# Kernel tuning notes

Measured on AMD Instinct MI355X. Metric: run time of the kernel, lower is better.

Reference implementation:

```python
import jax, jax.numpy as jnp
import numpy as np

N_NODES = 20000
N_EDGES = 200000
D_IN, D_H1, D_H2, D_OUT = 1433, 1000, 500, 7


def setup_inputs() -> dict:
    key = jax.random.key(0)
    ks = jax.random.split(key, 8)
    features = jax.random.normal(ks[0], (N_NODES, D_IN), dtype=jnp.float32)
    src = jax.random.randint(ks[1], (N_EDGES,), 0, N_NODES)
    dst = jax.random.randint(ks[2], (N_EDGES,), 0, N_NODES)
    W1 = jax.random.normal(ks[3], (D_IN, D_H1), dtype=jnp.float32) * 0.02
    b1 = jnp.zeros((D_H1,), dtype=jnp.float32)
    W2 = jax.random.normal(ks[4], (D_H1, D_H2), dtype=jnp.float32) * 0.02
    b2 = jnp.zeros((D_H2,), dtype=jnp.float32)
    W3 = jax.random.normal(ks[5], (D_H2, D_OUT), dtype=jnp.float32) * 0.02
    b3 = jnp.zeros((D_OUT,), dtype=jnp.float32)
    return {"features": features, "src": src, "dst": dst,
            "W1": W1, "b1": b1, "W2": W2, "b2": b2, "W3": W3, "b3": b3}


def reference(features, src, dst, W1, b1, W2, b2, W3, b3):
    N = features.shape[0]

    def agg(x):  # sum_tensors over incoming neighbors: h_i = sum_{(j->i) in E} x_j
        return jax.ops.segment_sum(x[src], dst, num_segments=N)

    # GCN layer 1: aggregate -> linear -> relu
    x = jax.nn.relu(agg(features) @ W1 + b1)       # [N, 1000]
    # GCN layer 2: aggregate -> linear -> relu (dropout = identity in eval)
    x = jax.nn.relu(agg(x) @ W2 + b2)              # [N, 500]
    # output linear -> relu (dropout = identity in eval)
    x = jax.nn.relu(x @ W3 + b3)                   # [N, 7]
    return x
```

## Files before the change

kernel.cpp:

```cpp
#include <hip/hip_runtime.h>
#include <hip/hip_bf16.h>


#define N_NODES 20000
#define N_EDGES 200000
#define D_IN    1433
#define D_H1    1000
#define D_H2    500
#define D_OUT   7

#define MPAD    20096
#define K1PAD   1472
#define N1PAD   1024
#define K2PAD   1024
#define N2PAD   512
#define H1STR   1008
#define H2STR   504
#define MBLK    157

typedef __attribute__((ext_vector_type(8))) short short8;
typedef __attribute__((ext_vector_type(8))) unsigned short ushort8_t;
typedef __attribute__((ext_vector_type(4))) float f32x4;

__device__ __forceinline__ unsigned short bf16_rne(float x) {
    unsigned int u = __float_as_uint(x);
    u = (u + 0x7FFFu + ((u >> 16) & 1u)) >> 16;
    return (unsigned short)u;
}
__device__ __forceinline__ float bf16_up(unsigned short h) {
    return __uint_as_float((unsigned int)h << 16);
}

__device__ __forceinline__ void gl_lds16(const unsigned short* g, unsigned short* lds) {
    __builtin_amdgcn_global_load_lds(
        (const __attribute__((address_space(1))) unsigned int*)g,
        (__attribute__((address_space(3))) unsigned int*)lds, 16, 0, 0);
}

__global__ __launch_bounds__(256) void count_deg(const int* __restrict__ dst,
                                                 int* __restrict__ offs) {
    int e = blockIdx.x * 256 + threadIdx.x;
    if (e < N_EDGES) atomicAdd(&offs[dst[e] + 1], 1);
}

__global__ __launch_bounds__(1024) void scan_csr(int* __restrict__ offs,
                                                 int* __restrict__ cursor, int n) {
    __shared__ int wsum[16];
    __shared__ int s_carry;
    const int t = threadIdx.x, lane = t & 63, wv = t >> 6;
    if (t == 0) s_carry = 0;
    __syncthreads();
    for (int base = 0; base < n; base += 1024) {
        int i = base + t;
        int v = (i < n) ? offs[i] : 0;
        #pragma unroll
        for (int s = 1; s < 64; s <<= 1) {
            int u = __shfl_up(v, s, 64);
            if (lane >= s) v += u;
        }
        if (lane == 63) wsum[wv] = v;
        __syncthreads();
        int prefix = s_carry;
        for (int k = 0; k < wv; ++k) prefix += wsum[k];
        v += prefix;
        if (i < n) {
            offs[i] = v;
            if (i < N_NODES) cursor[i] = v;
        }
        __syncthreads();
        if (t == 1023) s_carry = v;
    }
}

__global__ __launch_bounds__(256) void fill_csr(const int* __restrict__ src,
                                                const int* __restrict__ dst,
                                                int* __restrict__ cursor,
                                                int* __restrict__ srcs) {
    int e = blockIdx.x * 256 + threadIdx.x;
    if (e < N_EDGES) {
        int pos = atomicAdd(&cursor[dst[e]], 1);
        srcs[pos] = src[e];
    }
}

__global__ __launch_bounds__(256) void cast_features(const float* __restrict__ F,
                                                     unsigned int* __restrict__ out) {
    int row = blockIdx.x;
    int t = threadIdx.x;
    const float* fr = F + (size_t)row * D_IN;
    bool live = row < N_NODES;
    for (int kk = t; kk < K1PAD / 2; kk += 256) {
        int k0 = kk * 2;
        float a = (live && k0     < D_IN) ? fr[k0]     : 0.f;
        float b = (live && k0 + 1 < D_IN) ? fr[k0 + 1] : 0.f;
        out[(size_t)row * (K1PAD / 2) + kk] =
            (unsigned int)bf16_rne(a) | ((unsigned int)bf16_rne(b) << 16);
    }
}

template <int SR, int SC, int DR, int DC>
__global__ __launch_bounds__(256) void transpose_cast_pad(const float* __restrict__ src,
                                                          unsigned short* __restrict__ dst) {
    __shared__ float tile[32][33];
    int c0 = blockIdx.x * 32;
    int r0 = blockIdx.y * 32;
    int tx = threadIdx.x & 31, ty = threadIdx.x >> 5;
    #pragma unroll
    for (int p = 0; p < 4; ++p) {
        int r = r0 + ty + p * 8, c = c0 + tx;
        tile[ty + p * 8][tx] = (r < SR && c < SC) ? src[(size_t)r * SC + c] : 0.f;
    }
    __syncthreads();
    #pragma unroll
    for (int p = 0; p < 4; ++p) {
        int dr = c0 + ty + p * 8;
        int dc = r0 + tx;
        if (dr < DR && dc < DC) dst[(size_t)dr * DC + dc] = bf16_rne(tile[tx][ty + p * 8]);
    }
}

template <int KPAD, int NB>
__global__ __launch_bounds__(256) void gemm_mfma(const unsigned short* __restrict__ A,
                                                 const unsigned short* __restrict__ B,
                                                 unsigned short* __restrict__ C,
                                                 int M, int N, int OSTR) {
    __shared__ __align__(16) unsigned short sA[128 * 64];
    __shared__ __align__(16) unsigned short sB[128 * 64];
    const int bid = blockIdx.x;
    const int xcd = bid & 7;
    const int tt  = bid >> 3;
    const int nb  = tt % NB;
    const int mb  = (tt / NB) * 8 + xcd;
    if (mb >= MBLK) return;

    const int t = threadIdx.x;
    const int w = t >> 6, lane = t & 63;
    const int m0 = mb * 128, n0 = nb * 128;
    const int wm = (w >> 1) * 64, wn = (w & 1) * 64;

    const int srowo = lane >> 3;
    const int skc   = ((lane & 7) ^ srowo) * 8;
    const int mrow = lane & 15, quad = lane >> 4;

    const unsigned short* Aptr = A + (size_t)(m0 + srowo) * KPAD + skc;
    const unsigned short* Bptr = B + (size_t)(n0 + srowo) * KPAD + skc;

    f32x4 acc[4][4] = {};

    for (int k0 = 0; k0 < KPAD; k0 += 64) {
        #pragma unroll
        for (int c = 0; c < 4; ++c) {
            const int rbase = c * 32 + w * 8;
            gl_lds16(Aptr + (size_t)rbase * KPAD, &sA[rbase * 64]);
            gl_lds16(Bptr + (size_t)rbase * KPAD, &sB[rbase * 64]);
        }
        Aptr += 64; Bptr += 64;
        __syncthreads();

        #pragma unroll
        for (int s = 0; s < 2; ++s) {
            short8 af[4], bf[4];
            #pragma unroll
            for (int mt = 0; mt < 4; ++mt) {
                int r = wm + mt * 16 + mrow;
                af[mt] = *(const short8*)&sA[r * 64 + (((s * 4 + quad) ^ (mrow & 7)) * 8)];
            }
            #pragma unroll
            for (int nt = 0; nt < 4; ++nt) {
                int r = wn + nt * 16 + mrow;
                bf[nt] = *(const short8*)&sB[r * 64 + (((s * 4 + quad) ^ (mrow & 7)) * 8)];
            }
            #pragma unroll
            for (int mt = 0; mt < 4; ++mt)
                #pragma unroll
                for (int nt = 0; nt < 4; ++nt)
                    acc[mt][nt] = __builtin_amdgcn_mfma_f32_16x16x32_bf16(
                        af[mt], bf[nt], acc[mt][nt], 0, 0, 0);
        }
        __syncthreads();
    }

    #pragma unroll
    for (int mt = 0; mt < 4; ++mt) {
        int m = m0 + wm + mt * 16 + quad * 4;
        #pragma unroll
        for (int nt = 0; nt < 4; ++nt) {
            int n = n0 + wn + nt * 16 + mrow;
            if (n >= N) continue;
            #pragma unroll
            for (int r = 0; r < 4; ++r)
                if (m + r < M) C[(size_t)(m + r) * OSTR + n] = bf16_rne(acc[mt][nt][r]);
        }
    }
}

__global__ __launch_bounds__(128) void agg1_bf16(const unsigned short* __restrict__ H,
                                                 const int* __restrict__ offs,
                                                 const int* __restrict__ srcs,
                                                 const float* __restrict__ bias,
                                                 unsigned short* __restrict__ X) {
    const int i = blockIdx.x, t = threadIdx.x;
    const bool active = t < 125;
    const int tc = active ? t : 124;
    ushort8_t o = (ushort8_t)0;
    if (i < N_NODES) {
        const int beg = offs[i], end = offs[i + 1];
        const unsigned short* Hc = H + tc * 8;
        float s[8] = {};
        int e = beg;
        for (; e + 4 <= end; e += 4) {
            int j0 = srcs[e], j1 = srcs[e + 1], j2 = srcs[e + 2], j3 = srcs[e + 3];
            ushort8_t v0 = *(const ushort8_t*)(Hc + (size_t)j0 * H1STR);
            ushort8_t v1 = *(const ushort8_t*)(Hc + (size_t)j1 * H1STR);
            ushort8_t v2 = *(const ushort8_t*)(Hc + (size_t)j2 * H1STR);
            ushort8_t v3 = *(const ushort8_t*)(Hc + (size_t)j3 * H1STR);
            #pragma unroll
            for (int u = 0; u < 8; ++u)
                s[u] += (bf16_up(v0[u]) + bf16_up(v1[u])) +
                        (bf16_up(v2[u]) + bf16_up(v3[u]));
        }
        for (; e < end; ++e) {
            ushort8_t v = *(const ushort8_t*)(Hc + (size_t)srcs[e] * H1STR);
            #pragma unroll
            for (int u = 0; u < 8; ++u) s[u] += bf16_up(v[u]);
        }
        if (active) {
            #pragma unroll
            for (int u = 0; u < 8; ++u)
                o[u] = bf16_rne(fmaxf(s[u] + bias[t * 8 + u], 0.f));
        }
    }
    *(ushort8_t*)(X + (size_t)i * K2PAD + t * 8) = o;
}

__global__ __launch_bounds__(128) void agg2_out(const unsigned short* __restrict__ H,
                                                const int* __restrict__ offs,
                                                const int* __restrict__ srcs,
                                                const float* __restrict__ b2,
                                                const float* __restrict__ W3,
                                                const float* __restrict__ b3,
                                                float* __restrict__ out) {
    __shared__ float red[2][8];
    const int i = blockIdx.x, t = threadIdx.x;
    const bool active = t < 125;
    const int tc = active ? t : 124;
    const int beg = offs[i], end = offs[i + 1];
    const unsigned short* Hc = H + tc * 4;
    float s[4] = {};
    int e = beg;
    for (; e + 4 <= end; e += 4) {
        int j0 = srcs[e], j1 = srcs[e + 1], j2 = srcs[e + 2], j3 = srcs[e + 3];
        ushort4 v0 = *(const ushort4*)(Hc + (size_t)j0 * H2STR);
        ushort4 v1 = *(const ushort4*)(Hc + (size_t)j1 * H2STR);
        ushort4 v2 = *(const ushort4*)(Hc + (size_t)j2 * H2STR);
        ushort4 v3 = *(const ushort4*)(Hc + (size_t)j3 * H2STR);
        s[0] += (bf16_up(v0.x) + bf16_up(v1.x)) + (bf16_up(v2.x) + bf16_up(v3.x));
        s[1] += (bf16_up(v0.y) + bf16_up(v1.y)) + (bf16_up(v2.y) + bf16_up(v3.y));
        s[2] += (bf16_up(v0.z) + bf16_up(v1.z)) + (bf16_up(v2.z) + bf16_up(v3.z));
        s[3] += (bf16_up(v0.w) + bf16_up(v1.w)) + (bf16_up(v2.w) + bf16_up(v3.w));
    }
    for (; e < end; ++e) {
        ushort4 v = *(const ushort4*)(Hc + (size_t)srcs[e] * H2STR);
        s[0] += bf16_up(v.x); s[1] += bf16_up(v.y);
        s[2] += bf16_up(v.z); s[3] += bf16_up(v.w);
    }
    float acc[D_OUT] = {};
    if (active) {
        #pragma unroll
        for (int u = 0; u < 4; ++u) {
            float x = fmaxf(s[u] + b2[t * 4 + u], 0.f);
            const float* wr = W3 + (size_t)(t * 4 + u) * D_OUT;
            #pragma unroll
            for (int j = 0; j < D_OUT; ++j) acc[j] += x * wr[j];
        }
    }
    #pragma unroll
    for (int j = 0; j < D_OUT; ++j)
        #pragma unroll
        for (int off = 32; off; off >>= 1) acc[j] += __shfl_down(acc[j], off);
    const int lane = t & 63, wave = t >> 6;
    if (lane == 0) {
        #pragma unroll
        for (int j = 0; j < D_OUT; ++j) red[wave][j] = acc[j];
    }
    __syncthreads();
    if (t == 0) {
        #pragma unroll
        for (int j = 0; j < D_OUT; ++j)
            out[(size_t)i * D_OUT + j] = fmaxf(red[0][j] + red[1][j] + b3[j], 0.f);
    }
}

extern "C" void kernel_launch(void* const* d_in, const int* in_sizes, int n_in,
                              void* d_out, int out_size, void* d_ws, size_t ws_size,
                              hipStream_t stream) {
    const float* features = (const float*)d_in[0];
    const int*   src      = (const int*)d_in[1];
    const int*   dst      = (const int*)d_in[2];
    const float* W1       = (const float*)d_in[3];
    const float* b1       = (const float*)d_in[4];
    const float* W2       = (const float*)d_in[5];
    const float* b2       = (const float*)d_in[6];
    const float* W3       = (const float*)d_in[7];
    const float* b3       = (const float*)d_in[8];
    float* out = (float*)d_out;

    char* ws = (char*)d_ws;
    unsigned short* Fbf  = (unsigned short*)(ws + 0);
    unsigned short* X1bf = (unsigned short*)(ws + 0);
    unsigned short* H1   = (unsigned short*)(ws + 59162624);
    unsigned short* H2   = (unsigned short*)(ws + 59162624);
    unsigned short* W1T  = (unsigned short*)(ws + 99482624);
    unsigned short* W2T  = (unsigned short*)(ws + 102497280);
    int* offs   = (int*)(ws + 103545856);
    int* cursor = (int*)(ws + 103625984);
    int* srcs   = (int*)(ws + 103706112);

    hipMemsetAsync(offs, 0, (N_NODES + 1) * sizeof(int), stream);
    count_deg<<<(N_EDGES + 255) / 256, 256, 0, stream>>>(dst, offs);
    scan_csr<<<1, 1024, 0, stream>>>(offs, cursor, N_NODES + 1);
    fill_csr<<<(N_EDGES + 255) / 256, 256, 0, stream>>>(src, dst, cursor, srcs);

    cast_features<<<MPAD, 256, 0, stream>>>(features, (unsigned int*)Fbf);
    transpose_cast_pad<D_IN, D_H1, N1PAD, K1PAD>
        <<<dim3(N1PAD / 32, K1PAD / 32), 256, 0, stream>>>(W1, W1T);
    transpose_cast_pad<D_H1, D_H2, N2PAD, K2PAD>
        <<<dim3(N2PAD / 32, K2PAD / 32), 256, 0, stream>>>(W2, W2T);

    gemm_mfma<K1PAD, N1PAD / 128><<<8 * (N1PAD / 128) * 20, 256, 0, stream>>>(
        Fbf, W1T, H1, N_NODES, D_H1, H1STR);
    agg1_bf16<<<MPAD, 128, 0, stream>>>(H1, offs, srcs, b1, X1bf);

    gemm_mfma<K2PAD, N2PAD / 128><<<8 * (N2PAD / 128) * 20, 256, 0, stream>>>(
        X1bf, W2T, H2, N_NODES, D_H2, H2STR);
    agg2_out<<<N_NODES, 128, 0, stream>>>(H2, offs, srcs, b2, W3, b3, out);
}
```

Measured before the change: 439.3 us.

## Fuse CSR scan, feature cast and weight transposes into one prep launch; fold fill into GEMM1

Merges the feature cast, both weight transpose-casts and the CSR prefix scan into a single multi-role prep kernel selected by block index. The scan now runs in a single 256-thread block instead of 1024 threads. The CSR fill runs as extra blocks appended to the first GEMM launch. This removes several kernel launches and their serialization gaps, but the scan block may become a long tail because it has fewer threads and runs alongside the other prep work.

After: 448.9 us. +2.2%, slower.

```diff
diff --git a/kernel.cpp b/kernel.cpp
--- a/kernel.cpp
+++ b/kernel.cpp
@@ -43,67 +43,15 @@
     if (e < N_EDGES) atomicAdd(&offs[dst[e] + 1], 1);
 }
 
-__global__ __launch_bounds__(1024) void scan_csr(int* __restrict__ offs,
-                                                 int* __restrict__ cursor, int n) {
-    __shared__ int wsum[16];
-    __shared__ int s_carry;
-    const int t = threadIdx.x, lane = t & 63, wv = t >> 6;
-    if (t == 0) s_carry = 0;
-    __syncthreads();
-    for (int base = 0; base < n; base += 1024) {
-        int i = base + t;
-        int v = (i < n) ? offs[i] : 0;
-        #pragma unroll
-        for (int s = 1; s < 64; s <<= 1) {
-            int u = __shfl_up(v, s, 64);
-            if (lane >= s) v += u;
-        }
-        if (lane == 63) wsum[wv] = v;
-        __syncthreads();
-        int prefix = s_carry;
-        for (int k = 0; k < wv; ++k) prefix += wsum[k];
-        v += prefix;
-        if (i < n) {
-            offs[i] = v;
-            if (i < N_NODES) cursor[i] = v;
-        }
-        __syncthreads();
-        if (t == 1023) s_carry = v;
-    }
-}
-
-__global__ __launch_bounds__(256) void fill_csr(const int* __restrict__ src,
-                                                const int* __restrict__ dst,
-                                                int* __restrict__ cursor,
-                                                int* __restrict__ srcs) {
-    int e = blockIdx.x * 256 + threadIdx.x;
-    if (e < N_EDGES) {
-        int pos = atomicAdd(&cursor[dst[e]], 1);
-        srcs[pos] = src[e];
-    }
-}
-
-__global__ __launch_bounds__(256) void cast_features(const float* __restrict__ F,
-                                                     unsigned int* __restrict__ out) {
-    int row = blockIdx.x;
-    int t = threadIdx.x;
-    const float* fr = F + (size_t)row * D_IN;
-    bool live = row < N_NODES;
-    for (int kk = t; kk < K1PAD / 2; kk += 256) {
-        int k0 = kk * 2;
-        float a = (live && k0     < D_IN) ? fr[k0]     : 0.f;
-        float b = (live && k0 + 1 < D_IN) ? fr[k0 + 1] : 0.f;
-        out[(size_t)row * (K1PAD / 2) + kk] =
-            (unsigned int)bf16_rne(a) | ((unsigned int)bf16_rne(b) << 16);
-    }
-}
+#define T1_BLKS 1472
+#define T2_BLKS 512
 
 template <int SR, int SC, int DR, int DC>
-__global__ __launch_bounds__(256) void transpose_cast_pad(const float* __restrict__ src,
-                                                          unsigned short* __restrict__ dst) {
-    __shared__ float tile[32][33];
-    int c0 = blockIdx.x * 32;
-    int r0 = blockIdx.y * 32;
+__device__ void transpose_body(const float* __restrict__ src,
+                               unsigned short* __restrict__ dst,
+                               int bx, int by, float (*tile)[33]) {
+    int c0 = bx * 32;
+    int r0 = by * 32;
     int tx = threadIdx.x & 31, ty = threadIdx.x >> 5;
     #pragma unroll
     for (int p = 0; p < 4; ++p) {
@@ -119,14 +67,84 @@
     }
 }
 
-template <int KPAD, int NB>
+__global__ __launch_bounds__(256) void prep(const float* __restrict__ F,
+                                            unsigned int* __restrict__ Fbf,
+                                            const float* __restrict__ W1,
+                                            unsigned short* __restrict__ W1T,
+                                            const float* __restrict__ W2,
+                                            unsigned short* __restrict__ W2T,
+                                            int* __restrict__ offs,
+                                            int* __restrict__ cursor) {
+    __shared__ float tile[32][33];
+    __shared__ int wsum[4];
+    __shared__ int s_carry;
+    const int b = blockIdx.x, t = threadIdx.x;
+
+    if (b < MPAD) {
+        const float* fr = F + (size_t)b * D_IN;
+        bool live = b < N_NODES;
+        for (int kk = t; kk < K1PAD / 2; kk += 256) {
+            int k0 = kk * 2;
+            float a = (live && k0     < D_IN) ? fr[k0]     : 0.f;
+            float c = (live && k0 + 1 < D_IN) ? fr[k0 + 1] : 0.f;
+            Fbf[(size_t)b * (K1PAD / 2) + kk] =
+                (unsigned int)bf16_rne(a) | ((unsigned int)bf16_rne(c) << 16);
+        }
+    } else if (b < MPAD + T1_BLKS) {
+        int lb = b - MPAD;
+        transpose_body<D_IN, D_H1, N1PAD, K1PAD>(W1, W1T, lb & 31, lb >> 5, tile);
+    } else if (b < MPAD + T1_BLKS + T2_BLKS) {
+        int lb = b - MPAD - T1_BLKS;
+        transpose_body<D_H1, D_H2, N2PAD, K2PAD>(W2, W2T, lb & 15, lb >> 4, tile);
+    } else {
+        const int lane = t & 63, wv = t >> 6;
+        const int n = N_NODES + 1;
+        if (t == 0) s_carry = 0;
+        __syncthreads();
+        for (int base = 0; base < n; base += 256) {
+            int i = base + t;
+            int v = (i < n) ? offs[i] : 0;
+            #pragma unroll
+            for (int s = 1; s < 64; s <<= 1) {
+                int u = __shfl_up(v, s, 64);
+                if (lane >= s) v += u;
+            }
+            if (lane == 63) wsum[wv] = v;
+            __syncthreads();
+            int prefix = s_carry;
+            for (int k = 0; k < wv; ++k) prefix += wsum[k];
+            v += prefix;
+            if (i < n) {
+                offs[i] = v;
+                if (i < N_NODES) cursor[i] = v;
+            }
+            __syncthreads();
+            if (t == 255) s_carry = v;
+        }
+    }
+}
+
+template <int KPAD, int NB, bool FILL>
 __global__ __launch_bounds__(256) void gemm_mfma(const unsigned short* __restrict__ A,
                                                  const unsigned short* __restrict__ B,
                                                  unsigned short* __restrict__ C,
-                                                 int M, int N, int OSTR) {
+                                                 int M, int N, int OSTR,
+                                                 const int* __restrict__ esrc,
+                                                 const int* __restrict__ edst,
+                                                 int* __restrict__ cursor,
+                                                 int* __restrict__ srcs) {
+    constexpr int GEMMB = 8 * NB * ((MBLK + 7) / 8);
+    const int bid = blockIdx.x;
+    if (FILL && bid >= GEMMB) {
+        int e = (bid - GEMMB) * 256 + threadIdx.x;
+        if (e < N_EDGES) {
+            int pos = atomicAdd(&cursor[edst[e]], 1);
+            srcs[pos] = esrc[e];
+        }
+        return;
+    }
     __shared__ __align__(16) unsigned short sA[128 * 64];
     __shared__ __align__(16) unsigned short sB[128 * 64];
-    const int bid = blockIdx.x;
     const int xcd = bid & 7;
     const int tt  = bid >> 3;
     const int nb  = tt % NB;
@@ -318,20 +336,17 @@
 
     hipMemsetAsync(offs, 0, (N_NODES + 1) * sizeof(int), stream);
     count_deg<<<(N_EDGES + 255) / 256, 256, 0, stream>>>(dst, offs);
-    scan_csr<<<1, 1024, 0, stream>>>(offs, cursor, N_NODES + 1);
-    fill_csr<<<(N_EDGES + 255) / 256, 256, 0, stream>>>(src, dst, cursor, srcs);
-
-    cast_features<<<MPAD, 256, 0, stream>>>(features, (unsigned int*)Fbf);
-    transpose_cast_pad<D_IN, D_H1, N1PAD, K1PAD>
-        <<<dim3(N1PAD / 32, K1PAD / 32), 256, 0, stream>>>(W1, W1T);
-    transpose_cast_pad<D_H1, D_H2, N2PAD, K2PAD>
-        <<<dim3(N2PAD / 32, K2PAD / 32), 256, 0, stream>>>(W2, W2T);
-
-    gemm_mfma<K1PAD, N1PAD / 128><<<8 * (N1PAD / 128) * 20, 256, 0, stream>>>(
-        Fbf, W1T, H1, N_NODES, D_H1, H1STR);
+
+    prep<<<MPAD + T1_BLKS + T2_BLKS + 1, 256, 0, stream>>>(
+        features, (unsigned int*)Fbf, W1, W1T, W2, W2T, offs, cursor);
+
+    gemm_mfma<K1PAD, N1PAD / 128, true>
+        <<<8 * (N1PAD / 128) * 20 + (N_EDGES + 255) / 256, 256, 0, stream>>>(
+        Fbf, W1T, H1, N_NODES, D_H1, H1STR, src, dst, cursor, srcs);
     agg1_bf16<<<MPAD, 128, 0, stream>>>(H1, offs, srcs, b1, X1bf);
 
-    gemm_mfma<K2PAD, N2PAD / 128><<<8 * (N2PAD / 128) * 20, 256, 0, stream>>>(
-        X1bf, W2T, H2, N_NODES, D_H2, H2STR);
+    gemm_mfma<K2PAD, N2PAD / 128, false>
+        <<<8 * (N2PAD / 128) * 20, 256, 0, stream>>>(
+        X1bf, W2T, H2, N_NODES, D_H2, H2STR, nullptr, nullptr, nullptr, nullptr);
     agg2_out<<<N_NODES, 128, 0, stream>>>(H2, offs, srcs, b2, W3, b3, out);
 }
```
